# Optimization experiments

Measured on AMD Instinct MI355X. Metric: run time of the kernel, lower is better.

The kernel has to match this reference:

```python
import jax, jax.numpy as jnp
import numpy as np

VOCAB = 100000
EMB = 128
D = 8
K = 128
SUB = EMB // D  # 16
BN_EPS = 1e-3  # keras BatchNormalization default epsilon


def setup_inputs() -> dict:
    key = jax.random.key(0)
    k1, k2, k3 = jax.random.split(key, 3)
    ids = jax.random.randint(k1, (1024, 128), 0, VOCAB, dtype=jnp.int64)
    query_wemb = jax.random.normal(k2, (VOCAB, EMB), dtype=jnp.float32)
    centroids = jax.random.normal(k3, (D, K, SUB), dtype=jnp.float32)
    return {"ids": ids, "query_wemb": query_wemb, "centroids": centroids}


def reference(ids, query_wemb, centroids):
    d, k, sub = centroids.shape
    emb = d * sub
    flat = ids.reshape(-1)                      # [N]
    x = query_wemb[flat].reshape(-1, d, sub)    # [N, d, sub]

    norm_x = jnp.sum(x * x, axis=-1, keepdims=True)          # [N, d, 1]
    norm_c = jnp.sum(centroids * centroids, axis=-1)[None]   # [1, d, k]
    dot = jnp.einsum('nds,dks->ndk', x, centroids)           # [N, d, k]
    response = -norm_x + 2.0 * dot - norm_c                  # [N, d, k]

    # BatchNorm(scale=False, center=False), training=True: batch stats over
    # axes (0,1), per-k channel (keras default axis=-1)
    mean = jnp.mean(response, axis=(0, 1), keepdims=True)
    var = jnp.var(response, axis=(0, 1), keepdims=True)
    resp_bn = (response - mean) * jax.lax.rsqrt(var + BN_EPS)

    codes = jnp.argmax(resp_bn, axis=-1)                     # [N, d]

    # per-subspace centroid gather (non-shared centroids)
    outputs = centroids[jnp.arange(d)[None, :], codes]       # [N, d, sub]

    # straight-through estimator
    out_st = x + jax.lax.stop_gradient(outputs - x)          # [N, d, sub]
    return out_st.reshape(ids.shape + (emb,))
```

## Files before the change

### kernel.cpp

```cpp
#include <hip/hip_runtime.h>


constexpr int NTOK = 131072;
constexpr int ST   = 2320;
constexpr float EPS = 0.001f;

typedef float v2f __attribute__((ext_vector_type(2)));


__global__ __launch_bounds__(256) void k1_stats(const int* __restrict__ ids,
                                                const float* __restrict__ wemb,
                                                float* __restrict__ partials,
                                                int tpb)
{
    __shared__ float xs[32][132];
    __shared__ float nrm[32][8];
    const int t = threadIdx.x;
    const int b = blockIdx.x;

    float g[4][4];
#pragma unroll
    for (int i = 0; i < 4; ++i)
#pragma unroll
        for (int j = 0; j < 4; ++j) g[i][j] = 0.f;
    float sx = 0.f, hh = 0.f, s2 = 0.f;

    const int d_g = t >> 4;
    const int r0  = ((t >> 2) & 3) << 2;
    const int c0  = (t & 3) << 2;
    const int u   = t & 127;
    const int d_s = u >> 4;
    const int s_s = u & 15;

    const int nchunks = tpb >> 5;
    for (int ch = 0; ch < nchunks; ++ch) {
        const int n0 = b * tpb + ch * 32;
#pragma unroll
        for (int rep = 0; rep < 4; ++rep) {
            int i = t + rep * 256;
            int n = i >> 5, f = i & 31;
            int id = ids[n0 + n];
            float4 v = *(const float4*)(wemb + (size_t)id * 128 + f * 4);
            *(float4*)(&xs[n][f * 4]) = v;
        }
        __syncthreads();
        {
            int n = t >> 3, dd = t & 7;
            const float* xp = &xs[n][dd * 16];
            float4 a = *(const float4*)(xp);
            float4 bq = *(const float4*)(xp + 4);
            float4 c = *(const float4*)(xp + 8);
            float4 dq = *(const float4*)(xp + 12);
            float acc = a.x*a.x + a.y*a.y + a.z*a.z + a.w*a.w;
            acc += bq.x*bq.x + bq.y*bq.y + bq.z*bq.z + bq.w*bq.w;
            acc += c.x*c.x + c.y*c.y + c.z*c.z + c.w*c.w;
            acc += dq.x*dq.x + dq.y*dq.y + dq.z*dq.z + dq.w*dq.w;
            nrm[n][dd] = acc;
        }
        __syncthreads();
        if (t < 128) {
            for (int n = 0; n < 32; ++n) {
                const float* xp = &xs[n][d_g * 16];
                float4 av = *(const float4*)(xp + r0);
                float4 bv = *(const float4*)(xp + c0);
                float aa[4] = {av.x, av.y, av.z, av.w};
                float bb[4] = {bv.x, bv.y, bv.z, bv.w};
#pragma unroll
                for (int i = 0; i < 4; ++i)
#pragma unroll
                    for (int j = 0; j < 4; ++j)
                        g[i][j] = fmaf(aa[i], bb[j], g[i][j]);
            }
        } else {
            for (int n = 0; n < 32; ++n) {
                float xv = xs[n][d_s * 16 + s_s];
                float nv = nrm[n][d_s];
                sx += xv;
                hh = fmaf(nv, xv, hh);
                if (s_s == 0) s2 = fmaf(nv, nv, s2);
            }
        }
        __syncthreads();
    }
    float* pb = partials + (size_t)b * ST;
    if (t < 128) {
        const int base = d_g * 256;
#pragma unroll
        for (int i = 0; i < 4; ++i)
#pragma unroll
            for (int j = 0; j < 4; ++j)
                pb[base + (r0 + i) * 16 + (c0 + j)] = g[i][j];
    } else {
        pb[2048 + d_s * 16 + s_s] = sx;
        pb[2176 + d_s * 16 + s_s] = hh;
        if (s_s == 0) pb[2304 + d_s] = s2;
    }
}

__global__ __launch_bounds__(256) void k2a_reduce(float* __restrict__ partials, int nb)
{
    const int idx = blockIdx.x * 256 + threadIdx.x;
    if (idx >= 2312) return;
    const int y = blockIdx.y;
    float acc[8] = {0.f, 0.f, 0.f, 0.f, 0.f, 0.f, 0.f, 0.f};
    int b = y;
    while (b + 7 * 32 < nb) {
#pragma unroll
        for (int u = 0; u < 8; ++u)
            acc[u] += partials[(size_t)(b + u * 32) * ST + idx];
        b += 8 * 32;
    }
    while (b < nb) { acc[0] += partials[(size_t)b * ST + idx]; b += 32; }
    float s = ((acc[0] + acc[1]) + (acc[2] + acc[3]))
            + ((acc[4] + acc[5]) + (acc[6] + acc[7]));
    partials[(size_t)y * ST + idx] = s;
}

__global__ __launch_bounds__(256) void k2b_reduce(const float* __restrict__ partials,
                                                  float* __restrict__ stats)
{
    const int idx = blockIdx.x * 256 + threadIdx.x;
    if (idx >= 2312) return;
    float acc[8] = {0.f, 0.f, 0.f, 0.f, 0.f, 0.f, 0.f, 0.f};
#pragma unroll
    for (int j = 0; j < 4; ++j)
#pragma unroll
        for (int u = 0; u < 8; ++u)
            acc[u] += partials[(size_t)(j * 8 + u) * ST + idx];
    stats[idx] = ((acc[0] + acc[1]) + (acc[2] + acc[3]))
               + ((acc[4] + acc[5]) + (acc[6] + acc[7]));
}

__global__ __launch_bounds__(128) void k3_final(const float* __restrict__ stats,
                                                const float* __restrict__ centroids,
                                                float2* __restrict__ ab)
{
    __shared__ float st[2312];
    const int t = threadIdx.x;
    for (int i = t; i < 2312; i += 128) st[i] = stats[i];
    __syncthreads();
    const int k = t;

    double Sn[8], Sn_tot = 0.0, S2_tot = 0.0;
#pragma unroll
    for (int d = 0; d < 8; ++d) {
        double s = 0.0;
        for (int ss = 0; ss < 16; ++ss) s += (double)st[d * 256 + ss * 17];
        Sn[d] = s; Sn_tot += s;
        S2_tot += (double)st[2304 + d];
    }
    double sr = -Sn_tot, sr2 = S2_tot;
    double ncd[8];
    for (int d = 0; d < 8; ++d) {
        const float* cp = centroids + d * 2048 + k * 16;
        float cv[16];
#pragma unroll
        for (int s = 0; s < 16; ++s) cv[s] = cp[s];
        double nc = 0, cdSx = 0, ch = 0, cGc = 0;
        for (int s = 0; s < 16; ++s) {
            nc   += (double)cv[s] * cv[s];
            cdSx += (double)cv[s] * st[2048 + d * 16 + s];
            ch   += (double)cv[s] * st[2176 + d * 16 + s];
            double rd = 0;
            for (int s2i = 0; s2i < 16; ++s2i)
                rd += (double)st[d * 256 + s * 16 + s2i] * cv[s2i];
            cGc += (double)cv[s] * rd;
        }
        ncd[d] = nc;
        sr  += 2.0 * cdSx - (double)NTOK * nc;
        sr2 += 4.0 * cGc + (double)NTOK * nc * nc + 2.0 * nc * Sn[d]
               - 4.0 * ch - 4.0 * nc * cdSx;
    }
    const double M = (double)NTOK * 8.0;
    double mean = sr / M;
    double var  = sr2 / M - mean * mean;
    float alpha = (float)(1.0 / sqrt(var + (double)EPS));
#pragma unroll
    for (int d = 0; d < 8; ++d) {
        float beta = (float)((double)alpha * (-ncd[d] - mean));
        ab[d * 128 + k] = make_float2(2.f * alpha, beta);
    }
}

__global__ __launch_bounds__(256, 4) void k4_main(const int* __restrict__ ids,
                                                  const float* __restrict__ wemb,
                                                  const float* __restrict__ centroids,
                                                  const float2* __restrict__ ab,
                                                  float* __restrict__ out)
{
    __shared__ float2 gbs[128];

    const int t = threadIdx.x;
    const int d = blockIdx.y;
    const float* cd = centroids + (size_t)d * 2048;

    const float* cdv = cd;
    asm("" : "+v"(cdv));

    if (t < 128) gbs[t] = ab[(size_t)d * 128 + t];

    const int nbase = blockIdx.x * 1024 + t;
    v2f x[4][8];
    v2f nxv[4];
    float best[4];
    int   code[4];
#pragma unroll
    for (int j = 0; j < 4; ++j) {
        const int n = nbase + j * 256;
        const float* xp = wemb + (size_t)ids[n] * 128 + d * 16;
        float s = 0.f;
#pragma unroll
        for (int q = 0; q < 4; ++q) {
            float4 v = *(const float4*)(xp + q * 4);
            x[j][q * 2]     = (v2f){v.x, v.y};
            x[j][q * 2 + 1] = (v2f){v.z, v.w};
            s += v.x * v.x + v.y * v.y + v.z * v.z + v.w * v.w;
        }
        nxv[j] = (v2f){-0.5f * s, 0.f};
        best[j] = -3.4e38f;
        code[j] = 0;
    }

    __syncthreads();

#pragma unroll 2
    for (int k = 0; k < 128; ++k) {
        const float4 c0 = *(const float4*)(cdv + k * 16 + 0);
        const float4 c1 = *(const float4*)(cdv + k * 16 + 4);
        const float4 c2 = *(const float4*)(cdv + k * 16 + 8);
        const float4 c3 = *(const float4*)(cdv + k * 16 + 12);
        const float2 g  = gbs[k];
        const v2f cc0 = (v2f){c0.x, c0.y}, cc1 = (v2f){c0.z, c0.w};
        const v2f cc2 = (v2f){c1.x, c1.y}, cc3 = (v2f){c1.z, c1.w};
        const v2f cc4 = (v2f){c2.x, c2.y}, cc5 = (v2f){c2.z, c2.w};
        const v2f cc6 = (v2f){c3.x, c3.y}, cc7 = (v2f){c3.z, c3.w};
#pragma unroll
        for (int j = 0; j < 4; ++j) {
            v2f a = __builtin_elementwise_fma(cc0, x[j][0], nxv[j]);
            a = __builtin_elementwise_fma(cc1, x[j][1], a);
            a = __builtin_elementwise_fma(cc2, x[j][2], a);
            a = __builtin_elementwise_fma(cc3, x[j][3], a);
            a = __builtin_elementwise_fma(cc4, x[j][4], a);
            a = __builtin_elementwise_fma(cc5, x[j][5], a);
            a = __builtin_elementwise_fma(cc6, x[j][6], a);
            a = __builtin_elementwise_fma(cc7, x[j][7], a);
            float acc = a[0] + a[1];
            float sc = fmaf(g.x, acc, g.y);
            bool p = sc > best[j];
            best[j] = p ? sc : best[j];
            code[j] = p ? k : code[j];
        }
    }

#pragma unroll
    for (int j = 0; j < 4; ++j) {
        const int n = nbase + j * 256;
        const float* cw = cd + code[j] * 16;
        float* op = out + (size_t)n * 128 + d * 16;
#pragma unroll
        for (int q = 0; q < 4; ++q) {
            float4 cv = *(const float4*)(cw + q * 4);
            float x0 = x[j][q * 2][0],     x1 = x[j][q * 2][1];
            float x2 = x[j][q * 2 + 1][0], x3 = x[j][q * 2 + 1][1];
            float4 o;
            o.x = x0 + (cv.x - x0);
            o.y = x1 + (cv.y - x1);
            o.z = x2 + (cv.z - x2);
            o.w = x3 + (cv.w - x3);
            *(float4*)(op + q * 4) = o;
        }
    }
}

extern "C" void kernel_launch(void* const* d_in, const int* in_sizes, int n_in,
                              void* d_out, int out_size, void* d_ws, size_t ws_size,
                              hipStream_t stream)
{
    const int* ids    = (const int*)d_in[0];
    const float* wemb = (const float*)d_in[1];
    const float* cent = (const float*)d_in[2];
    float* out = (float*)d_out;
    float* ws  = (float*)d_ws;

    int p1b = 1024;
    if (ws_size < ((size_t)1024 * ST + 2320 + 2048) * 4) p1b = 512;
    if (ws_size < ((size_t)512  * ST + 2320 + 2048) * 4) p1b = 256;
    if (ws_size < ((size_t)256  * ST + 2320 + 2048) * 4) p1b = 128;
    const int tpb = NTOK / p1b;

    float* partials = ws;
    float* stats    = ws + (size_t)p1b * ST;
    float2* ab      = (float2*)(stats + 2320);

    hipLaunchKernelGGL(k1_stats,   dim3(p1b),     dim3(256), 0, stream, ids, wemb, partials, tpb);
    hipLaunchKernelGGL(k2a_reduce, dim3(10, 32),  dim3(256), 0, stream, partials, p1b);
    hipLaunchKernelGGL(k2b_reduce, dim3(10),      dim3(256), 0, stream, partials, stats);
    hipLaunchKernelGGL(k3_final,   dim3(1),       dim3(128), 0, stream, stats, cent, ab);
    hipLaunchKernelGGL(k4_main,    dim3(128, 8),  dim3(256), 0, stream, ids, wemb, cent, ab, out);
}
```

Before: 147.3 us.

## Stage centroids in LDS, broadcast BN coefficients via readlane, double stats blocks

```diff
diff --git a/kernel.cpp b/kernel.cpp
--- a/kernel.cpp
+++ b/kernel.cpp
@@ -6,6 +6,10 @@
 constexpr float EPS = 0.001f;
 
 typedef float v2f __attribute__((ext_vector_type(2)));
+
+__device__ inline float rlane(float v, int lane) {
+    return __int_as_float(__builtin_amdgcn_readlane(__float_as_int(v), lane));
+}
 
 
 __global__ __launch_bounds__(256) void k1_stats(const int* __restrict__ ids,
@@ -188,16 +192,19 @@
                                                   const float2* __restrict__ ab,
                                                   float* __restrict__ out)
 {
-    __shared__ float2 gbs[128];
+    __shared__ float cs[128 * 16];
 
     const int t = threadIdx.x;
     const int d = blockIdx.y;
+    const int lane = t & 63;
     const float* cd = centroids + (size_t)d * 2048;
 
-    const float* cdv = cd;
-    asm("" : "+v"(cdv));
-
-    if (t < 128) gbs[t] = ab[(size_t)d * 128 + t];
+#pragma unroll
+    for (int i = 0; i < 2; ++i)
+        ((float4*)cs)[t + i * 256] = ((const float4*)cd)[t + i * 256];
+
+    const float2 g_lo = ab[(size_t)d * 128 + lane];
+    const float2 g_hi = ab[(size_t)d * 128 + 64 + lane];
 
     const int nbase = blockIdx.x * 1024 + t;
     v2f x[4][8];
@@ -223,34 +230,41 @@
 
     __syncthreads();
 
-#pragma unroll 2
-    for (int k = 0; k < 128; ++k) {
-        const float4 c0 = *(const float4*)(cdv + k * 16 + 0);
-        const float4 c1 = *(const float4*)(cdv + k * 16 + 4);
-        const float4 c2 = *(const float4*)(cdv + k * 16 + 8);
-        const float4 c3 = *(const float4*)(cdv + k * 16 + 12);
-        const float2 g  = gbs[k];
-        const v2f cc0 = (v2f){c0.x, c0.y}, cc1 = (v2f){c0.z, c0.w};
-        const v2f cc2 = (v2f){c1.x, c1.y}, cc3 = (v2f){c1.z, c1.w};
-        const v2f cc4 = (v2f){c2.x, c2.y}, cc5 = (v2f){c2.z, c2.w};
-        const v2f cc6 = (v2f){c3.x, c3.y}, cc7 = (v2f){c3.z, c3.w};
-#pragma unroll
-        for (int j = 0; j < 4; ++j) {
-            v2f a = __builtin_elementwise_fma(cc0, x[j][0], nxv[j]);
-            a = __builtin_elementwise_fma(cc1, x[j][1], a);
-            a = __builtin_elementwise_fma(cc2, x[j][2], a);
-            a = __builtin_elementwise_fma(cc3, x[j][3], a);
-            a = __builtin_elementwise_fma(cc4, x[j][4], a);
-            a = __builtin_elementwise_fma(cc5, x[j][5], a);
-            a = __builtin_elementwise_fma(cc6, x[j][6], a);
-            a = __builtin_elementwise_fma(cc7, x[j][7], a);
-            float acc = a[0] + a[1];
-            float sc = fmaf(g.x, acc, g.y);
-            bool p = sc > best[j];
-            best[j] = p ? sc : best[j];
-            code[j] = p ? k : code[j];
-        }
-    }
+#define KHALF(GSRC, KOFF)                                                    \
+    _Pragma("unroll 2")                                                      \
+    for (int k = 0; k < 64; ++k) {                                           \
+        const int kk = k + (KOFF);                                           \
+        const float4 c0 = *(const float4*)(&cs[kk * 16 + 0]);                \
+        const float4 c1 = *(const float4*)(&cs[kk * 16 + 4]);                \
+        const float4 c2 = *(const float4*)(&cs[kk * 16 + 8]);                \
+        const float4 c3 = *(const float4*)(&cs[kk * 16 + 12]);               \
+        const float ga_ = rlane(GSRC.x, k);                                  \
+        const float gb_ = rlane(GSRC.y, k);                                  \
+        const v2f cc0 = (v2f){c0.x, c0.y}, cc1 = (v2f){c0.z, c0.w};          \
+        const v2f cc2 = (v2f){c1.x, c1.y}, cc3 = (v2f){c1.z, c1.w};          \
+        const v2f cc4 = (v2f){c2.x, c2.y}, cc5 = (v2f){c2.z, c2.w};          \
+        const v2f cc6 = (v2f){c3.x, c3.y}, cc7 = (v2f){c3.z, c3.w};          \
+        _Pragma("unroll")                                                    \
+        for (int j = 0; j < 4; ++j) {                                        \
+            v2f a = __builtin_elementwise_fma(cc0, x[j][0], nxv[j]);         \
+            a = __builtin_elementwise_fma(cc1, x[j][1], a);                  \
+            a = __builtin_elementwise_fma(cc2, x[j][2], a);                  \
+            a = __builtin_elementwise_fma(cc3, x[j][3], a);                  \
+            a = __builtin_elementwise_fma(cc4, x[j][4], a);                  \
+            a = __builtin_elementwise_fma(cc5, x[j][5], a);                  \
+            a = __builtin_elementwise_fma(cc6, x[j][6], a);                  \
+            a = __builtin_elementwise_fma(cc7, x[j][7], a);                  \
+            float acc = a[0] + a[1];                                         \
+            float sc = fmaf(ga_, acc, gb_);                                  \
+            bool p = sc > best[j];             \
+            best[j] = p ? sc : best[j];                                      \
+            code[j] = p ? kk : code[j];                                      \
+        }                                                                    \
+    }
+
+    KHALF(g_lo, 0)
+    KHALF(g_hi, 64)
+#undef KHALF
 
 #pragma unroll
     for (int j = 0; j < 4; ++j) {
@@ -282,7 +296,8 @@
     float* out = (float*)d_out;
     float* ws  = (float*)d_ws;
 
-    int p1b = 1024;
+    int p1b = 2048;
+    if (ws_size < ((size_t)2048 * ST + 2320 + 2048) * 4) p1b = 1024;
     if (ws_size < ((size_t)1024 * ST + 2320 + 2048) * 4) p1b = 512;
     if (ws_size < ((size_t)512  * ST + 2320 + 2048) * 4) p1b = 256;
     if (ws_size < ((size_t)256  * ST + 2320 + 2048) * 4) p1b = 128;
```

After: 127.5 us. 1.16x faster.
